# Kernel tuning notes

Hardware: AMD Instinct MI355X
Metric: run time of the kernel (lower is better)

## Reference

```python
import jax, jax.numpy as jnp
import numpy as np

DEGREE = 7

def setup_inputs() -> dict:
    key = jax.random.key(0)
    k1, k2 = jax.random.split(key)
    input_dims, output_dims = 1024, 1024
    x = jax.random.normal(k1, (8192, input_dims), dtype=jnp.float32)
    std = 1.0 / (input_dims * (DEGREE + 1))
    lucas_coeffs = std * jax.random.normal(k2, (input_dims, output_dims, DEGREE + 1), dtype=jnp.float32)
    return {"x": x, "lucas_coeffs": lucas_coeffs}

def reference(x, lucas_coeffs):
    input_dims = lucas_coeffs.shape[0]
    x = x.reshape(-1, input_dims)
    x = jnp.tanh(x)
    # Lucas polynomial recurrence: L0=2, L1=x, L_i = x*L_{i-1} + L_{i-2}
    basis = [jnp.full_like(x, 2.0)]
    if DEGREE > 0:
        basis.append(x)
    for i in range(2, DEGREE + 1):
        basis.append(x * basis[-1] + basis[-2])
    lucas = jnp.stack(basis, axis=-1)  # [b, i, d]
    y = jnp.einsum('bid,iod->bo', lucas, lucas_coeffs)
    return y
```

## Files before the change

kernel.cpp:

```cpp
#include <hip/hip_runtime.h>
#include <hip/hip_bf16.h>


typedef __attribute__((ext_vector_type(8)))  short  short8;
typedef __attribute__((ext_vector_type(4)))  unsigned short ushort4v;
typedef __attribute__((ext_vector_type(8)))  unsigned short ushort8;
typedef __attribute__((ext_vector_type(4)))  float  float4v;
typedef __attribute__((ext_vector_type(16))) float  float16v;
typedef __attribute__((ext_vector_type(4)))  unsigned int uint4v;

#define M_DIM 8192
#define I_DIM 1024
#define O_DIM 1024
#define K_DIM 8192
#define BM 128
#define BN 128
#define BK 64
#define KSPLIT 2
#define KHALF (K_DIM / KSPLIT)
#define NSTEP (KHALF / BK)

__device__ __forceinline__ unsigned short f2bf(float f) {
    unsigned int u = __float_as_uint(f);
    u += 0x7FFFu + ((u >> 16) & 1u);
    return (unsigned short)(u >> 16);
}

__global__ __launch_bounds__(256) void prep_kernel(const float* __restrict__ x,
                                                   const float* __restrict__ c,
                                                   unsigned short* __restrict__ T,
                                                   unsigned short* __restrict__ Bt,
                                                   float* __restrict__ outz) {
    const int zPart = (M_DIM * O_DIM) / (4 * 256);
    const int tPart = (M_DIM * I_DIM) / (8 * 256);
    int bid = blockIdx.x;
    int tid = threadIdx.x;
    if (bid < zPart) {
        int idx = (bid * 256 + tid) * 4;
        const float4v z = {0.f, 0.f, 0.f, 0.f};
        *(float4v*)(outz + idx) = z;
    } else if (bid < zPart + tPart) {
        int idx = ((bid - zPart) * 256 + tid) * 8;
        float4v v0 = *(const float4v*)(x + idx);
        float4v v1 = *(const float4v*)(x + idx + 4);
        unsigned short t[8];
        t[0] = f2bf(tanhf(v0[0])); t[1] = f2bf(tanhf(v0[1]));
        t[2] = f2bf(tanhf(v0[2])); t[3] = f2bf(tanhf(v0[3]));
        t[4] = f2bf(tanhf(v1[0])); t[5] = f2bf(tanhf(v1[1]));
        t[6] = f2bf(tanhf(v1[2])); t[7] = f2bf(tanhf(v1[3]));
        ushort8 o;
        #pragma unroll
        for (int p = 0; p < 4; ++p) { o[p] = t[2 * p]; o[4 + p] = t[2 * p + 1]; }
        *(ushort8*)(T + idx) = o;
    } else {
        __shared__ unsigned short S[32][64 * 8 + 8];
        int tb = bid - zPart - tPart;
        const int i0 = (tb >> 5) * 64;
        const int o0 = (tb & 31) * 32;
        #pragma unroll 4
        for (int p = 0; p < 16; ++p) {
            const int il = p * 4 + (tid >> 6);
            const int e  = (tid & 63) * 4;
            const float* src = c + (size_t)(i0 + il) * 8192 + o0 * 8 + e;
            float4v v = *(const float4v*)src;
            ushort4v u;
            u[0] = f2bf(v[0]); u[1] = f2bf(v[1]); u[2] = f2bf(v[2]); u[3] = f2bf(v[3]);
            *(ushort4v*)&S[e >> 3][il * 8 + (e & 7)] = u;
        }
        __syncthreads();
        #pragma unroll 4
        for (int q = 0; q < 16; ++q) {
            const int ol = q * 2 + (tid >> 7);
            const int ch = (tid & 127) * 4;
            ushort4v u = *(const ushort4v*)&S[ol][ch];
            *(ushort4v*)(Bt + (size_t)(o0 + ol) * K_DIM + i0 * 8 + ch) = u;
        }
    }
}

__device__ __forceinline__ short8 lucas_frag(unsigned int tb) {
    const float t = __uint_as_float(tb << 16);
    const float L2v = fmaf(t, t, 2.0f);
    const float L3v = fmaf(t, L2v, t);
    const float L4v = fmaf(t, L3v, L2v);
    const float L5v = fmaf(t, L4v, L3v);
    const float L6v = fmaf(t, L5v, L4v);
    const float L7v = fmaf(t, L6v, L5v);
    union { uint4v u; short8 s; } r;
#if __has_builtin(__builtin_amdgcn_cvt_pk_bf16_f32)
    {
        auto p0 = __builtin_amdgcn_cvt_pk_bf16_f32(2.0f, t);
        auto p1 = __builtin_amdgcn_cvt_pk_bf16_f32(L2v, L3v);
        auto p2 = __builtin_amdgcn_cvt_pk_bf16_f32(L4v, L5v);
        auto p3 = __builtin_amdgcn_cvt_pk_bf16_f32(L6v, L7v);
        __builtin_memcpy(&r.u[0], &p0, 4);
        __builtin_memcpy(&r.u[1], &p1, 4);
        __builtin_memcpy(&r.u[2], &p2, 4);
        __builtin_memcpy(&r.u[3], &p3, 4);
    }
#else
    {
        r.u[0] = 0x4000u | (tb << 16);
        r.u[1] = __builtin_amdgcn_perm(__float_as_uint(L3v), __float_as_uint(L2v), 0x07060302);
        r.u[2] = __builtin_amdgcn_perm(__float_as_uint(L5v), __float_as_uint(L4v), 0x07060302);
        r.u[3] = __builtin_amdgcn_perm(__float_as_uint(L7v), __float_as_uint(L6v), 0x07060302);
    }
#endif
    return r.s;
}

__global__ __launch_bounds__(256, 4) void gemm_kernel(const unsigned short* __restrict__ T,
                                                      const unsigned short* __restrict__ Bt,
                                                      float* __restrict__ out) {
    __shared__ unsigned short Bs[2][BN * BK];
    __shared__ unsigned short Ts[2][BM * 8];

    const int tid  = threadIdx.x;
    const int lane = tid & 63;
    const int wave = tid >> 6;
    const int n0 = blockIdx.x * BN;
    const int m0 = blockIdx.y * BM;
    const int k0 = blockIdx.z * KHALF;

    const int wm0 = (wave >> 1) * 64;
    const int wn0 = (wave & 1) * 64;
    const int l32 = lane & 31;
    const int h   = lane >> 5;

    const int srow   = lane >> 3;
    const int il     = lane & 7;
    const int gchunk = il ^ srow;

    float16v acc[2][2];
    #pragma unroll
    for (int a = 0; a < 2; ++a)
        #pragma unroll
        for (int b = 0; b < 2; ++b)
            #pragma unroll
            for (int e = 0; e < 16; ++e) acc[a][b][e] = 0.f;

    auto stage = [&](int buf, int kt) {
        #pragma unroll
        for (int r = 0; r < 4; ++r) {
            const int rowb = r * 32 + wave * 8;
            const unsigned short* gB = Bt + (size_t)(n0 + rowb + srow) * K_DIM + kt + gchunk * 8;
            __builtin_amdgcn_global_load_lds(
                (const __attribute__((address_space(1))) unsigned int*)gB,
                (__attribute__((address_space(3))) unsigned int*)&Bs[buf][rowb * BK], 16, 0, 0);
        }
        if (wave < 2) {
            const unsigned short* gT = T + (size_t)(m0 + wave * 64 + lane) * I_DIM + kt / 8;
            __builtin_amdgcn_global_load_lds(
                (const __attribute__((address_space(1))) unsigned int*)gT,
                (__attribute__((address_space(3))) unsigned int*)&Ts[buf][wave * 64 * 8], 16, 0, 0);
        }
    };

    stage(0, k0);
    __syncthreads();

    int cur = 0;
    for (int s = 0; s < NSTEP; ++s) {
        const int nxt = cur ^ 1;
        if (s + 1 < NSTEP) stage(nxt, k0 + (s + 1) * BK);

        unsigned long long tw[2];
        #pragma unroll
        for (int tt = 0; tt < 2; ++tt)
            tw[tt] = *(const unsigned long long*)&Ts[cur][(wm0 + tt * 32 + l32) * 8 + h * 4];

        #pragma unroll
        for (int kk = 0; kk < 4; ++kk) {
            short8 bfr[2];
            #pragma unroll
            for (int tn = 0; tn < 2; ++tn) {
                const int brow = wn0 + tn * 32 + l32;
                bfr[tn] = *(const short8*)&Bs[cur][brow * BK + (((kk * 2 + h) ^ (brow & 7)) * 8)];
            }
            #pragma unroll
            for (int tt = 0; tt < 2; ++tt) {
                const short8 af = lucas_frag((unsigned int)((tw[tt] >> (16 * kk)) & 0xffffu));
                #pragma unroll
                for (int tn = 0; tn < 2; ++tn)
                    acc[tt][tn] = __builtin_amdgcn_mfma_f32_32x32x16_bf16(
                        af, bfr[tn], acc[tt][tn], 0, 0, 0);
            }
        }

        __syncthreads();
        cur = nxt;
    }

    #pragma unroll
    for (int tt = 0; tt < 2; ++tt) {
        #pragma unroll
        for (int tn = 0; tn < 2; ++tn) {
            const int col = n0 + wn0 + tn * 32 + l32;
            #pragma unroll
            for (int reg = 0; reg < 16; ++reg) {
                const int row = m0 + wm0 + tt * 32 + (reg & 3) + 8 * (reg >> 2) + 4 * h;
                atomicAdd(&out[(size_t)row * O_DIM + col], acc[tt][tn][reg]);
            }
        }
    }
}

__global__ __launch_bounds__(256) void naive_kernel(const float* __restrict__ x,
                                                    const float* __restrict__ c,
                                                    float* __restrict__ out) {
    int idx = blockIdx.x * 256 + threadIdx.x;
    int b = idx >> 10;
    int o = idx & 1023;
    const float* xb = x + (size_t)b * I_DIM;
    float acc = 0.f;
    for (int i = 0; i < I_DIM; ++i) {
        float t = tanhf(xb[i]);
        float L[8];
        L[0] = 2.0f; L[1] = t;
        #pragma unroll
        for (int d = 2; d < 8; ++d) L[d] = t * L[d - 1] + L[d - 2];
        const float* cc = c + (size_t)i * 8192 + o * 8;
        #pragma unroll
        for (int d = 0; d < 8; ++d) acc += L[d] * cc[d];
    }
    out[idx] = acc;
}

extern "C" void kernel_launch(void* const* d_in, const int* in_sizes, int n_in,
                              void* d_out, int out_size, void* d_ws, size_t ws_size,
                              hipStream_t stream) {
    const float* x      = (const float*)d_in[0];
    const float* coeffs = (const float*)d_in[1];
    float* out = (float*)d_out;

    const size_t btBytes = (size_t)O_DIM * K_DIM * sizeof(unsigned short);
    const size_t tBytes  = (size_t)M_DIM * I_DIM * sizeof(unsigned short);

    if (ws_size >= btBytes + tBytes) {
        unsigned short* Bt = (unsigned short*)d_ws;
        unsigned short* T  = (unsigned short*)((char*)d_ws + btBytes);

        const int zBlocks = (M_DIM * O_DIM) / (4 * 256);
        const int tBlocks = (M_DIM * I_DIM) / (8 * 256);
        const int xBlocks = (I_DIM / 64) * (I_DIM / 32);
        prep_kernel<<<zBlocks + tBlocks + xBlocks, 256, 0, stream>>>(x, coeffs, T, Bt, out);

        dim3 grid(O_DIM / BN, M_DIM / BM, KSPLIT);
        gemm_kernel<<<grid, 256, 0, stream>>>(T, Bt, out);
    } else {
        naive_kernel<<<(M_DIM * O_DIM) / 256, 256, 0, stream>>>(x, coeffs, out);
    }
}
```

Baseline: 259.3 us.

## Switch GEMM to 16x16x32 MFMA with per-wave 32-row strips

Replaces the 32x32x16 bf16 MFMA tiling (2x2 waves of 64x64) with 16x16x32 MFMA where each wave owns a 32-row strip across all 128 columns. The packed tanh layout in T is re-interleaved to match the new A-fragment lane mapping, so each lane reads one 32-bit word per tile instead of 64 bits. The aim is fewer Lucas fragment constructions per MFMA and a different LDS access pattern for B. In exchange, each wave now reads all 128 B rows from LDS rather than 64, which doubles B LDS traffic per wave.

```diff
diff --git a/kernel.cpp b/kernel.cpp
--- a/kernel.cpp
+++ b/kernel.cpp
@@ -6,7 +6,6 @@
 typedef __attribute__((ext_vector_type(4)))  unsigned short ushort4v;
 typedef __attribute__((ext_vector_type(8)))  unsigned short ushort8;
 typedef __attribute__((ext_vector_type(4)))  float  float4v;
-typedef __attribute__((ext_vector_type(16))) float  float16v;
 typedef __attribute__((ext_vector_type(4)))  unsigned int uint4v;
 
 #define M_DIM 8192
@@ -50,7 +49,7 @@
         t[6] = f2bf(tanhf(v1[2])); t[7] = f2bf(tanhf(v1[3]));
         ushort8 o;
         #pragma unroll
-        for (int p = 0; p < 4; ++p) { o[p] = t[2 * p]; o[4 + p] = t[2 * p + 1]; }
+        for (int p = 0; p < 4; ++p) { o[2 * p] = t[p]; o[2 * p + 1] = t[p + 4]; }
         *(ushort8*)(T + idx) = o;
     } else {
         __shared__ unsigned short S[32][64 * 8 + 8];
@@ -122,22 +121,20 @@
     const int m0 = blockIdx.y * BM;
     const int k0 = blockIdx.z * KHALF;
 
-    const int wm0 = (wave >> 1) * 64;
-    const int wn0 = (wave & 1) * 64;
-    const int l32 = lane & 31;
-    const int h   = lane >> 5;
+    const int wm0  = wave * 32;
+    const int l16  = lane & 15;
+    const int quad = lane >> 4;
 
     const int srow   = lane >> 3;
     const int il     = lane & 7;
     const int gchunk = il ^ srow;
 
-    float16v acc[2][2];
+    float4v acc[2][8];
+    const float4v zero = {0.f, 0.f, 0.f, 0.f};
     #pragma unroll
     for (int a = 0; a < 2; ++a)
         #pragma unroll
-        for (int b = 0; b < 2; ++b)
-            #pragma unroll
-            for (int e = 0; e < 16; ++e) acc[a][b][e] = 0.f;
+        for (int b = 0; b < 8; ++b) acc[a][b] = zero;
 
     auto stage = [&](int buf, int kt) {
         #pragma unroll
@@ -164,26 +161,30 @@
         const int nxt = cur ^ 1;
         if (s + 1 < NSTEP) stage(nxt, k0 + (s + 1) * BK);
 
-        unsigned long long tw[2];
+        unsigned int tw[2];
         #pragma unroll
         for (int tt = 0; tt < 2; ++tt)
-            tw[tt] = *(const unsigned long long*)&Ts[cur][(wm0 + tt * 32 + l32) * 8 + h * 4];
-
-        #pragma unroll
-        for (int kk = 0; kk < 4; ++kk) {
-            short8 bfr[2];
+            tw[tt] = *(const unsigned int*)&Ts[cur][(wm0 + tt * 16 + l16) * 8 + quad * 2];
+
+        #pragma unroll
+        for (int k2 = 0; k2 < 2; ++k2) {
+            short8 af[2];
+            af[0] = lucas_frag(k2 ? (tw[0] >> 16) : (tw[0] & 0xffffu));
+            af[1] = lucas_frag(k2 ? (tw[1] >> 16) : (tw[1] & 0xffffu));
             #pragma unroll
-            for (int tn = 0; tn < 2; ++tn) {
-                const int brow = wn0 + tn * 32 + l32;
-                bfr[tn] = *(const short8*)&Bs[cur][brow * BK + (((kk * 2 + h) ^ (brow & 7)) * 8)];
-            }
-            #pragma unroll
-            for (int tt = 0; tt < 2; ++tt) {
-                const short8 af = lucas_frag((unsigned int)((tw[tt] >> (16 * kk)) & 0xffffu));
+            for (int g = 0; g < 2; ++g) {
+                short8 bfr[4];
                 #pragma unroll
-                for (int tn = 0; tn < 2; ++tn)
-                    acc[tt][tn] = __builtin_amdgcn_mfma_f32_32x32x16_bf16(
-                        af, bfr[tn], acc[tt][tn], 0, 0, 0);
+                for (int j = 0; j < 4; ++j) {
+                    const int brow = (g * 4 + j) * 16 + l16;
+                    bfr[j] = *(const short8*)&Bs[cur][brow * BK + (((k2 * 4 + quad) ^ (l16 & 7)) * 8)];
+                }
+                #pragma unroll
+                for (int tt = 0; tt < 2; ++tt)
+                    #pragma unroll
+                    for (int j = 0; j < 4; ++j)
+                        acc[tt][g * 4 + j] = __builtin_amdgcn_mfma_f32_16x16x32_bf16(
+                            af[tt], bfr[j], acc[tt][g * 4 + j], 0, 0, 0);
             }
         }
 
@@ -194,12 +195,12 @@
     #pragma unroll
     for (int tt = 0; tt < 2; ++tt) {
         #pragma unroll
-        for (int tn = 0; tn < 2; ++tn) {
-            const int col = n0 + wn0 + tn * 32 + l32;
+        for (int tn = 0; tn < 8; ++tn) {
+            const int col = n0 + tn * 16 + l16;
             #pragma unroll
-            for (int reg = 0; reg < 16; ++reg) {
-                const int row = m0 + wm0 + tt * 32 + (reg & 3) + 8 * (reg >> 2) + 4 * h;
-                atomicAdd(&out[(size_t)row * O_DIM + col], acc[tt][tn][reg]);
+            for (int r = 0; r < 4; ++r) {
+                const int row = m0 + wm0 + tt * 16 + quad * 4 + r;
+                atomicAdd(&out[(size_t)row * O_DIM + col], acc[tt][tn][r]);
             }
         }
     }
```

Result: faster. 247.8 us (-4.4%).
